# Kernel tuning notes

Measured on AMD Instinct MI355X. Metric: run time of the kernel, lower is better.

## Reference

```python
import jax, jax.numpy as jnp
import numpy as np

B = 64          # number of jets
LVLS = 13       # tree levels (complete binary tree, 4096 leaves/jet)
F = 7           # input features
H = 64          # hidden size
SIZES = [B * (2 ** j) for j in range(LVLS)]
OFFS = np.concatenate([[0], np.cumsum(SIZES)])  # level offsets into flat contents


def setup_inputs() -> dict:
    key = jax.random.key(0)
    ks = jax.random.split(key, 9)
    n_total = int(OFFS[-1])  # 524224
    s = lambda k, shp, fan: jax.random.normal(k, shp, jnp.float32) / np.sqrt(fan)
    return {
        "contents": jax.random.normal(ks[0], (n_total, F), jnp.float32),
        "W_u": s(ks[1], (H, F), F),       "b_u": jnp.zeros((H,), jnp.float32),
        "W_r": s(ks[2], (3 * H, 3 * H), 3 * H), "b_r": jnp.zeros((3 * H,), jnp.float32),
        "W_h": s(ks[3], (H, 3 * H), 3 * H),     "b_h": jnp.zeros((H,), jnp.float32),
        "W_z": s(ks[4], (4 * H, 4 * H), 4 * H), "b_z": jnp.zeros((4 * H,), jnp.float32),
    }


def reference(contents, W_u, b_u, W_r, b_r, W_h, b_h, W_z, b_z):
    # Bottom-up recursive gated embedding (n_iters=0 path -> relu activation).
    up = None  # embedding of level j+1
    for j in reversed(range(LVLS)):
        c = contents[int(OFFS[j]):int(OFFS[j + 1])]        # [n_j, F]
        u = jax.nn.relu(c @ W_u.T + b_u)                   # [n_j, H]
        if j == LVLS - 1:
            up = u                                         # leaf level: no inners
            continue
        n = SIZES[j]
        # children of node k are (2k, 2k+1) at level j+1 -> strided gather
        h_L = up[0::2]                                     # [n_j, H]
        h_R = up[1::2]                                     # [n_j, H]
        hhu = jnp.concatenate([h_L, h_R, u], axis=1)       # [n_j, 3H]
        r = jax.nn.sigmoid(hhu @ W_r.T + b_r)              # reset gate
        h_H = jax.nn.relu((r * hhu) @ W_h.T + b_h)         # candidate
        z = jnp.concatenate([h_H, hhu], axis=1) @ W_z.T + b_z  # [n_j, 4H]
        g = jax.nn.softmax(z.reshape(n, 4, H), axis=1)     # softmax over 4 gates
        up = g[:, 0] * h_H + g[:, 1] * h_L + g[:, 2] * h_R + g[:, 3] * u
    return up.reshape(B, -1)                               # [B, H]
```

## Files before the change

### kernel.cpp

```cpp
#include <hip/hip_runtime.h>
#include <hip/hip_bf16.h>


#define LOG2E 1.4426950408889634f
#define OSTR 76

typedef __bf16 bf16x8 __attribute__((ext_vector_type(8)));
typedef float f32x4 __attribute__((ext_vector_type(4)));
typedef unsigned short bfr;

__device__ __forceinline__ float bfr2f(bfr v) { return __uint_as_float(((unsigned)v) << 16); }
__device__ __forceinline__ bfr f2bfr(float f) {
    __hip_bfloat16 h = __float2bfloat16(f);
    return __builtin_bit_cast(bfr, h);
}
__device__ __forceinline__ float fexp2(float x) {
#if __has_builtin(__builtin_amdgcn_exp2f)
    return __builtin_amdgcn_exp2f(x);
#else
    return exp2f(x);
#endif
}
__device__ __forceinline__ float frcp(float x) {
#if __has_builtin(__builtin_amdgcn_rcpf)
    return __builtin_amdgcn_rcpf(x);
#else
    return 1.f / x;
#endif
}

__device__ __forceinline__ int fidx(int Mt, int kt, int q, int ln, int KT) {
    return ((((Mt * KT + kt) * 4 + q) * 16 + ln) * 8);
}

__device__ __host__ __forceinline__ size_t lvloff(int j) {
    return (size_t)((64 << j) - 64) * 64;
}

__device__ __forceinline__ void pack_one(const float* __restrict__ W, bfr* __restrict__ dst,
                                         int d, int K, float scale) {
    int KT = K >> 5;
    int j = d & 7, lnc = (d >> 3) & 15, q = (d >> 7) & 3;
    int t1 = d >> 9;
    int kt = t1 % KT, ntile = t1 / KT;
    int ncol = ntile * 16 + lnc;
    int k = kt * 32 + q * 8 + j;
    dst[d] = f2bfr(W[(size_t)ncol * K + k] * scale);
}

__global__ void convert_weights(const float* __restrict__ Wr, const float* __restrict__ Wh,
                                const float* __restrict__ Wz, const float* __restrict__ Wu,
                                const float* __restrict__ br, const float* __restrict__ bz,
                                bfr* __restrict__ wr, bfr* __restrict__ wh, bfr* __restrict__ wz,
                                bfr* __restrict__ wu,
                                float* __restrict__ brs, float* __restrict__ bzs) {
    int i = blockIdx.x * 256 + threadIdx.x;
    if (i < 36864) pack_one(Wr, wr, i, 192, LOG2E);
    if (i < 12288) pack_one(Wh, wh, i, 192, 1.f);
    if (i < 65536) pack_one(Wz, wz, i, 256, LOG2E);
    if (i < 2048) {
        int j = i & 7, lnc = (i >> 3) & 15, q = (i >> 7) & 3, ntile = i >> 9;
        int k = q * 8 + j, ncol = ntile * 16 + lnc;
        wu[i] = (k < 7) ? f2bfr(Wu[ncol * 7 + k]) : (bfr)0;
    }
    if (i < 192) brs[i] = br[i] * LOG2E;
    if (i < 256) bzs[i] = bz[i] * LOG2E;
}

__device__ __forceinline__ void stage_c(const float* __restrict__ csrc, int rows,
                                        bfr* s_c) {
    const int tid = threadIdx.x;
    for (int t = tid; t < rows * 4; t += 256) {
        int row = t >> 2, qg = t & 3;
        ushort v[8] = {0, 0, 0, 0, 0, 0, 0, 0};
        if (qg == 0) {
            const float* cp = csrc + (size_t)row * 7;
#pragma unroll
            for (int k = 0; k < 7; ++k) v[k] = f2bfr(cp[k]);
        }
        *(uint4*)&s_c[(((row >> 4) * 4 + qg) * 16 + (row & 15)) * 8] = *(const uint4*)v;
    }
}

__device__ __forceinline__ void store_up_coalesced(
    int row0, int rows, bfr* __restrict__ u_io,
    const ushort (&ovv)[4][4], int Mtn, bfr* s_t)
{
    const int tid = threadIdx.x;
    const int lane = tid & 63, w = tid >> 6;
    const int ln = lane & 15, q = lane >> 4;
    const int colbase = w * 16 + q * 4;
    __syncthreads();
#pragma unroll
    for (int Mt = 0; Mt < 4; ++Mt) {
        if (Mt < Mtn) {
            int row = Mt * 16 + ln;
            if (row < rows)
                *(uint2*)&s_t[row * OSTR + colbase] = *(const uint2*)ovv[Mt];
        }
    }
    __syncthreads();
#pragma unroll
    for (int it = 0; it < 2; ++it) {
        int idx = it * 256 + tid;
        int row = idx >> 3, ck = idx & 7;
        if (row < rows)
            *(uint4*)&u_io[(size_t)(row0 + row) * 64 + ck * 8] =
                *(const uint4*)&s_t[row * OSTR + ck * 8];
    }
}

__device__ __forceinline__ void mmu_own(const bfr* s_c, bfr* s_hhu, bf16x8 awu,
                                        f32x4 bu4, int Mtn, int ln, int q,
                                        int colbase) {
#pragma unroll
    for (int Mt = 0; Mt < 4; ++Mt) {
        if (Mt < Mtn) {
            bf16x8 Bc = *(const bf16x8*)&s_c[((Mt * 4 + q) * 16 + ln) * 8];
            f32x4 acc = {0.f, 0.f, 0.f, 0.f};
            acc = __builtin_amdgcn_mfma_f32_16x16x32_bf16(awu, Bc, acc, 0, 0, 0);
            int kk = 128 + colbase;
            int addr = fidx(Mt, kk >> 5, (kk >> 3) & 3, ln, 6) + (kk & 7);
            ushort uv[4];
#pragma unroll
            for (int r = 0; r < 4; ++r) uv[r] = f2bfr(fmaxf(acc[r] + bu4[r], 0.f));
            *(uint2*)&s_hhu[addr] = *(const uint2*)uv;
        }
    }
}

template <bool CHILD_U>
__device__ __forceinline__ void process_level_glob(
    int row0,
    const bfr* __restrict__ ch, const float* __restrict__ c_child,
    const float* __restrict__ c_own, bfr* __restrict__ u_io,
    const bfr* __restrict__ wu, const float* __restrict__ b_u,
    const bfr* __restrict__ wr, const float* __restrict__ brs,
    const bfr* __restrict__ wh, const float* __restrict__ b_h,
    const bfr* __restrict__ wz, const float* __restrict__ bzs,
    bfr* s_hhu, bfr* s_t)
{
    bfr* s_hH = s_t;
    const int tid = threadIdx.x;
    const int lane = tid & 63, w = tid >> 6;
    const int ln = lane & 15, q = lane >> 4;
    const int colbase = w * 16 + q * 4;
    const int rows = 64, Mtn = 4;

    if (!CHILD_U) {
#pragma unroll
        for (int it = 0; it < 4; ++it) {
            int idx = it * 256 + tid;
            int lns = idx & 15, qs = (idx >> 4) & 3, kts = (idx >> 6) & 3, Mts = idx >> 8;
            int row = Mts * 16 + lns;
            int k = kts * 32 + qs * 8;
            const bfr* src = (k < 64)
                ? ch + (size_t)(2 * (row0 + row)) * 64 + k
                : ch + (size_t)(2 * (row0 + row) + 1) * 64 + (k - 64);
            *(uint4*)&s_hhu[fidx(Mts, kts, qs, lns, 6)] = *(const uint4*)src;
        }
    } else {
        stage_c(c_child + (size_t)(2 * row0) * 7, 128, s_t + 2048);
    }
    stage_c(c_own + (size_t)row0 * 7, 64, s_t);
    __syncthreads();

    {
        bf16x8 awu = *(const bf16x8*)&wu[fidx(w, 0, q, ln, 1)];
        f32x4 bu4 = *(const f32x4*)&b_u[colbase];
        if (CHILD_U) {
#pragma unroll
            for (int Mt = 0; Mt < 8; ++Mt) {
                bf16x8 Bc = *(const bf16x8*)&s_t[2048 + (((Mt * 4 + q) * 16 + ln) * 8)];
                f32x4 acc = {0.f, 0.f, 0.f, 0.f};
                acc = __builtin_amdgcn_mfma_f32_16x16x32_bf16(awu, Bc, acc, 0, 0, 0);
                int crow = Mt * 16 + ln;
                int row = crow >> 1;
                int kk = (crow & 1) * 64 + colbase;
                int addr = fidx(row >> 4, kk >> 5, (kk >> 3) & 3, row & 15, 6) + (kk & 7);
                ushort uv[4];
#pragma unroll
                for (int r = 0; r < 4; ++r) uv[r] = f2bfr(fmaxf(acc[r] + bu4[r], 0.f));
                *(uint2*)&s_hhu[addr] = *(const uint2*)uv;
            }
        }
        mmu_own(s_t, s_hhu, awu, bu4, 4, ln, q, colbase);
    }
    __syncthreads();

    {
        bf16x8 Af[3][6];
#pragma unroll
        for (int nt = 0; nt < 3; ++nt)
#pragma unroll
            for (int kt = 0; kt < 6; ++kt)
                Af[nt][kt] = *(const bf16x8*)&wr[fidx(w * 3 + nt, kt, q, ln, 6)];
#pragma unroll
        for (int Mt = 0; Mt < 4; ++Mt) {
            bf16x8 Bf[6];
#pragma unroll
            for (int kt = 0; kt < 6; ++kt)
                Bf[kt] = *(const bf16x8*)&s_hhu[fidx(Mt, kt, q, ln, 6)];
#pragma unroll
            for (int nt = 0; nt < 3; ++nt) {
                int cb1 = (w * 3 + nt) * 16 + q * 4;
                f32x4 acc = {0.f, 0.f, 0.f, 0.f};
#pragma unroll
                for (int kt = 0; kt < 6; ++kt)
                    acc = __builtin_amdgcn_mfma_f32_16x16x32_bf16(Af[nt][kt], Bf[kt], acc, 0, 0, 0);
                f32x4 br4 = *(const f32x4*)&brs[cb1];
                int addr = fidx(Mt, cb1 >> 5, (cb1 >> 3) & 3, ln, 6) + (cb1 & 7);
                ushort hh[4], tt[4];
                *(uint2*)hh = *(const uint2*)&s_hhu[addr];
#pragma unroll
                for (int r = 0; r < 4; ++r) {
                    float e = fexp2(-(acc[r] + br4[r]));
                    tt[r] = f2bfr(frcp(1.f + e) * bfr2f(hh[r]));
                }
                *(uint2*)&s_t[addr] = *(const uint2*)tt;
            }
        }
    }
    __syncthreads();

    f32x4 hacc[4];
    {
        bf16x8 Ah[6];
#pragma unroll
        for (int kt = 0; kt < 6; ++kt)
            Ah[kt] = *(const bf16x8*)&wh[fidx(w, kt, q, ln, 6)];
#pragma unroll
        for (int Mt = 0; Mt < 4; ++Mt) {
            f32x4 acc = {0.f, 0.f, 0.f, 0.f};
#pragma unroll
            for (int kt = 0; kt < 6; ++kt) {
                bf16x8 Bf = *(const bf16x8*)&s_t[fidx(Mt, kt, q, ln, 6)];
                acc = __builtin_amdgcn_mfma_f32_16x16x32_bf16(Ah[kt], Bf, acc, 0, 0, 0);
            }
            hacc[Mt] = acc;
        }
    }
    __syncthreads();
    {
        f32x4 bh4 = *(const f32x4*)&b_h[colbase];
#pragma unroll
        for (int Mt = 0; Mt < 4; ++Mt) {
            int addr = fidx(Mt, colbase >> 5, (colbase >> 3) & 3, ln, 2) + (colbase & 7);
            ushort hv[4];
#pragma unroll
            for (int r = 0; r < 4; ++r) hv[r] = f2bfr(fmaxf(hacc[Mt][r] + bh4[r], 0.f));
            *(uint2*)&s_hH[addr] = *(const uint2*)hv;
        }
    }
    __syncthreads();

    {
        f32x4 az[4][4];
#pragma unroll
        for (int Mt = 0; Mt < 4; ++Mt)
#pragma unroll
            for (int g = 0; g < 4; ++g) az[Mt][g] = (f32x4){0.f, 0.f, 0.f, 0.f};
#pragma unroll
        for (int g = 0; g < 4; ++g) {
            bf16x8 Aw[8];
#pragma unroll
            for (int kt = 0; kt < 8; ++kt)
                Aw[kt] = *(const bf16x8*)&wz[fidx(g * 4 + w, kt, q, ln, 8)];
#pragma unroll
            for (int Mt = 0; Mt < 4; ++Mt) {
                f32x4 acc = az[Mt][g];
                acc = __builtin_amdgcn_mfma_f32_16x16x32_bf16(
                    Aw[0], *(const bf16x8*)&s_hH[fidx(Mt, 0, q, ln, 2)], acc, 0, 0, 0);
                acc = __builtin_amdgcn_mfma_f32_16x16x32_bf16(
                    Aw[1], *(const bf16x8*)&s_hH[fidx(Mt, 1, q, ln, 2)], acc, 0, 0, 0);
#pragma unroll
                for (int kt = 0; kt < 6; ++kt)
                    acc = __builtin_amdgcn_mfma_f32_16x16x32_bf16(
                        Aw[2 + kt], *(const bf16x8*)&s_hhu[fidx(Mt, kt, q, ln, 6)], acc, 0, 0, 0);
                az[Mt][g] = acc;
            }
        }
        f32x4 bz0 = *(const f32x4*)&bzs[colbase];
        f32x4 bz1 = *(const f32x4*)&bzs[64 + colbase];
        f32x4 bz2 = *(const f32x4*)&bzs[128 + colbase];
        f32x4 bz3 = *(const f32x4*)&bzs[192 + colbase];
        ushort ovv[4][4];
#pragma unroll
        for (int Mt = 0; Mt < 4; ++Mt) {
            int aH = fidx(Mt, colbase >> 5, (colbase >> 3) & 3, ln, 2) + (colbase & 7);
            int a0 = fidx(Mt, colbase >> 5, (colbase >> 3) & 3, ln, 6) + (colbase & 7);
            int c1 = 64 + colbase, c2 = 128 + colbase;
            int a1 = fidx(Mt, c1 >> 5, (c1 >> 3) & 3, ln, 6) + (c1 & 7);
            int a2 = fidx(Mt, c2 >> 5, (c2 >> 3) & 3, ln, 6) + (c2 & 7);
            ushort hHv[4], u0[4], u1[4], u2[4];
            *(uint2*)hHv = *(const uint2*)&s_hH[aH];
            *(uint2*)u0 = *(const uint2*)&s_hhu[a0];
            *(uint2*)u1 = *(const uint2*)&s_hhu[a1];
            *(uint2*)u2 = *(const uint2*)&s_hhu[a2];
#pragma unroll
            for (int r = 0; r < 4; ++r) {
                float e0 = fexp2(az[Mt][0][r] + bz0[r]);
                float e1 = fexp2(az[Mt][1][r] + bz1[r]);
                float e2 = fexp2(az[Mt][2][r] + bz2[r]);
                float e3 = fexp2(az[Mt][3][r] + bz3[r]);
                float inv = frcp(e0 + e1 + e2 + e3);
                float v = (e0 * bfr2f(hHv[r]) + e1 * bfr2f(u0[r]) +
                           e2 * bfr2f(u1[r]) + e3 * bfr2f(u2[r])) * inv;
                ovv[Mt][r] = f2bfr(v);
            }
        }
        store_up_coalesced(row0, rows, u_io, ovv, Mtn, s_t);
    }
}

__global__ __launch_bounds__(256, 2) void level11_kernel(
    const float* __restrict__ c12, const float* __restrict__ c11,
    bfr* __restrict__ u_io,
    const bfr* __restrict__ wr, const float* __restrict__ brs,
    const bfr* __restrict__ wh, const float* __restrict__ b_h,
    const bfr* __restrict__ wz, const float* __restrict__ bzs,
    const bfr* __restrict__ wu, const float* __restrict__ b_u)
{
    __shared__ bfr s_hhu[12288];
    __shared__ bfr s_t[12288];
    process_level_glob<true>(blockIdx.x * 64, nullptr, c12, c11, u_io,
                             wu, b_u, wr, brs, wh, b_h, wz, bzs, s_hhu, s_t);
}

__global__ __launch_bounds__(256, 2) void level_kernel(
    const bfr* __restrict__ ch, const float* __restrict__ c_own,
    bfr* __restrict__ u_io,
    const bfr* __restrict__ wr, const float* __restrict__ brs,
    const bfr* __restrict__ wh, const float* __restrict__ b_h,
    const bfr* __restrict__ wz, const float* __restrict__ bzs,
    const bfr* __restrict__ wu, const float* __restrict__ b_u)
{
    __shared__ bfr s_hhu[12288];
    __shared__ bfr s_t[12288];
    process_level_glob<false>(blockIdx.x * 64, ch, nullptr, c_own, u_io,
                              wu, b_u, wr, brs, wh, b_h, wz, bzs, s_hhu, s_t);
}

__device__ __forceinline__ void load_wregs(
    const bfr* __restrict__ wr, const bfr* __restrict__ wh, const bfr* __restrict__ wz,
    const bfr* __restrict__ wu, int w, int q, int ln,
    bf16x8 (&Af)[3][6], bf16x8 (&Ah)[6], bf16x8 (&Aw)[4][8], bf16x8& awu)
{
#pragma unroll
    for (int nt = 0; nt < 3; ++nt)
#pragma unroll
        for (int kt = 0; kt < 6; ++kt)
            Af[nt][kt] = *(const bf16x8*)&wr[fidx(w * 3 + nt, kt, q, ln, 6)];
#pragma unroll
    for (int kt = 0; kt < 6; ++kt)
        Ah[kt] = *(const bf16x8*)&wh[fidx(w, kt, q, ln, 6)];
#pragma unroll
    for (int g = 0; g < 4; ++g)
#pragma unroll
        for (int kt = 0; kt < 8; ++kt)
            Aw[g][kt] = *(const bf16x8*)&wz[fidx(g * 4 + w, kt, q, ln, 8)];
    awu = *(const bf16x8*)&wu[fidx(w, 0, q, ln, 1)];
}

__device__ __forceinline__ void process_level_regs(
    int row0, int rows,
    const bfr* __restrict__ ch, const float* __restrict__ c_own,
    bfr* __restrict__ u_io,
    const bf16x8 awu, const float* __restrict__ b_u,
    const bf16x8 (&Af)[3][6], const bf16x8 (&Ah)[6], const bf16x8 (&Aw)[4][8],
    const float* __restrict__ brs, const float* __restrict__ b_h,
    const float* __restrict__ bzs,
    float* __restrict__ outp, bfr* s_hhu, bfr* s_t)
{
    bfr* s_hH = s_t;
    const int tid = threadIdx.x;
    const int lane = tid & 63, w = tid >> 6;
    const int ln = lane & 15, q = lane >> 4;
    const int Mtn = (rows + 15) >> 4;
    const int colbase = w * 16 + q * 4;

    __syncthreads();

#pragma unroll
    for (int it = 0; it < 4; ++it) {
        int idx = it * 256 + tid;
        int lns = idx & 15, qs = (idx >> 4) & 3, kts = (idx >> 6) & 3, Mts = idx >> 8;
        int row = Mts * 16 + lns;
        if (row < rows) {
            int k = kts * 32 + qs * 8;
            const bfr* src = (k < 64)
                ? ch + (size_t)(2 * (row0 + row)) * 64 + k
                : ch + (size_t)(2 * (row0 + row) + 1) * 64 + (k - 64);
            *(uint4*)&s_hhu[fidx(Mts, kts, qs, lns, 6)] = *(const uint4*)src;
        }
    }
    stage_c(c_own + (size_t)row0 * 7, rows, s_t);
    __syncthreads();

    {
        f32x4 bu4 = *(const f32x4*)&b_u[colbase];
        mmu_own(s_t, s_hhu, awu, bu4, Mtn, ln, q, colbase);
    }
    __syncthreads();

#pragma unroll
    for (int Mt = 0; Mt < 4; ++Mt) {
        if (Mt < Mtn) {
            bf16x8 Bf[6];
#pragma unroll
            for (int kt = 0; kt < 6; ++kt)
                Bf[kt] = *(const bf16x8*)&s_hhu[fidx(Mt, kt, q, ln, 6)];
#pragma unroll
            for (int nt = 0; nt < 3; ++nt) {
                int cb1 = (w * 3 + nt) * 16 + q * 4;
                f32x4 acc = {0.f, 0.f, 0.f, 0.f};
#pragma unroll
                for (int kt = 0; kt < 6; ++kt)
                    acc = __builtin_amdgcn_mfma_f32_16x16x32_bf16(Af[nt][kt], Bf[kt], acc, 0, 0, 0);
                f32x4 br4 = *(const f32x4*)&brs[cb1];
                int addr = fidx(Mt, cb1 >> 5, (cb1 >> 3) & 3, ln, 6) + (cb1 & 7);
                ushort hh[4], tt[4];
                *(uint2*)hh = *(const uint2*)&s_hhu[addr];
#pragma unroll
                for (int r = 0; r < 4; ++r) {
                    float e = fexp2(-(acc[r] + br4[r]));
                    tt[r] = f2bfr(frcp(1.f + e) * bfr2f(hh[r]));
                }
                *(uint2*)&s_t[addr] = *(const uint2*)tt;
            }
        }
    }
    __syncthreads();

    f32x4 hacc[4];
#pragma unroll
    for (int Mt = 0; Mt < 4; ++Mt) {
        if (Mt < Mtn) {
            f32x4 acc = {0.f, 0.f, 0.f, 0.f};
#pragma unroll
            for (int kt = 0; kt < 6; ++kt) {
                bf16x8 Bf = *(const bf16x8*)&s_t[fidx(Mt, kt, q, ln, 6)];
                acc = __builtin_amdgcn_mfma_f32_16x16x32_bf16(Ah[kt], Bf, acc, 0, 0, 0);
            }
            hacc[Mt] = acc;
        }
    }
    __syncthreads();
    {
        f32x4 bh4 = *(const f32x4*)&b_h[colbase];
#pragma unroll
        for (int Mt = 0; Mt < 4; ++Mt) {
            if (Mt < Mtn) {
                int addr = fidx(Mt, colbase >> 5, (colbase >> 3) & 3, ln, 2) + (colbase & 7);
                ushort hv[4];
#pragma unroll
                for (int r = 0; r < 4; ++r) hv[r] = f2bfr(fmaxf(hacc[Mt][r] + bh4[r], 0.f));
                *(uint2*)&s_hH[addr] = *(const uint2*)hv;
            }
        }
    }
    __syncthreads();

    {
        f32x4 bz0 = *(const f32x4*)&bzs[colbase];
        f32x4 bz1 = *(const f32x4*)&bzs[64 + colbase];
        f32x4 bz2 = *(const f32x4*)&bzs[128 + colbase];
        f32x4 bz3 = *(const f32x4*)&bzs[192 + colbase];
        ushort ovv[4][4];
#pragma unroll
        for (int Mt = 0; Mt < 4; ++Mt) {
            if (Mt < Mtn) {
                bf16x8 Az[8];
                Az[0] = *(const bf16x8*)&s_hH[fidx(Mt, 0, q, ln, 2)];
                Az[1] = *(const bf16x8*)&s_hH[fidx(Mt, 1, q, ln, 2)];
#pragma unroll
                for (int kt = 0; kt < 6; ++kt)
                    Az[2 + kt] = *(const bf16x8*)&s_hhu[fidx(Mt, kt, q, ln, 6)];
                f32x4 azg[4];
#pragma unroll
                for (int g = 0; g < 4; ++g) {
                    f32x4 acc = {0.f, 0.f, 0.f, 0.f};
#pragma unroll
                    for (int kt = 0; kt < 8; ++kt)
                        acc = __builtin_amdgcn_mfma_f32_16x16x32_bf16(Aw[g][kt], Az[kt], acc, 0, 0, 0);
                    azg[g] = acc;
                }
                int aH = fidx(Mt, colbase >> 5, (colbase >> 3) & 3, ln, 2) + (colbase & 7);
                int a0 = fidx(Mt, colbase >> 5, (colbase >> 3) & 3, ln, 6) + (colbase & 7);
                int c1 = 64 + colbase, c2 = 128 + colbase;
                int a1 = fidx(Mt, c1 >> 5, (c1 >> 3) & 3, ln, 6) + (c1 & 7);
                int a2 = fidx(Mt, c2 >> 5, (c2 >> 3) & 3, ln, 6) + (c2 & 7);
                int row = Mt * 16 + ln;
                if (row < rows) {
                    ushort hHv[4], u0[4], u1[4], u2[4];
                    *(uint2*)hHv = *(const uint2*)&s_hH[aH];
                    *(uint2*)u0 = *(const uint2*)&s_hhu[a0];
                    *(uint2*)u1 = *(const uint2*)&s_hhu[a1];
                    *(uint2*)u2 = *(const uint2*)&s_hhu[a2];
                    float of[4];
#pragma unroll
                    for (int r = 0; r < 4; ++r) {
                        float e0 = fexp2(azg[0][r] + bz0[r]);
                        float e1 = fexp2(azg[1][r] + bz1[r]);
                        float e2 = fexp2(azg[2][r] + bz2[r]);
                        float e3 = fexp2(azg[3][r] + bz3[r]);
                        float inv = frcp(e0 + e1 + e2 + e3);
                        float v = (e0 * bfr2f(hHv[r]) + e1 * bfr2f(u0[r]) +
                                   e2 * bfr2f(u1[r]) + e3 * bfr2f(u2[r])) * inv;
                        ovv[Mt][r] = f2bfr(v); of[r] = v;
                    }
                    if (outp)
                        *(float4*)&outp[(size_t)(row0 + row) * 64 + colbase] = *(const float4*)of;
                }
            }
        }
        store_up_coalesced(row0, rows, u_io, ovv, Mtn, s_t);
    }
}

__global__ __launch_bounds__(256, 1) void fused_mid_regs(
    const float* __restrict__ contents, bfr* __restrict__ u_all,
    const bfr* __restrict__ wr, const float* __restrict__ brs,
    const bfr* __restrict__ wh, const float* __restrict__ b_h,
    const bfr* __restrict__ wz, const float* __restrict__ bzs,
    const bfr* __restrict__ wu, const float* __restrict__ b_u)
{
    __shared__ bfr s_hhu[12288];
    __shared__ bfr s_t[12288];
    const int tid = threadIdx.x;
    const int lane = tid & 63, w = tid >> 6, ln = lane & 15, q = lane >> 4;
    bf16x8 Af[3][6], Ah[6], Aw[4][8], awu;
    load_wregs(wr, wh, wz, wu, w, q, ln, Af, Ah, Aw, awu);
    for (int j = 8; j >= 2; --j) {
        int rows = 1 << (j - 2);
        const float* c_own = contents + (size_t)((64 << j) - 64) * 7;
        process_level_regs(blockIdx.x * rows, rows,
                           u_all + lvloff(j + 1), c_own, u_all + lvloff(j),
                           awu, b_u, Af, Ah, Aw, brs, b_h, bzs,
                           nullptr, s_hhu, s_t);
    }
}

__global__ __launch_bounds__(256, 1) void fused_tail_regs(
    const float* __restrict__ contents, bfr* __restrict__ u_all,
    const bfr* __restrict__ wr, const float* __restrict__ brs,
    const bfr* __restrict__ wh, const float* __restrict__ b_h,
    const bfr* __restrict__ wz, const float* __restrict__ bzs,
    const bfr* __restrict__ wu, const float* __restrict__ b_u,
    float* __restrict__ outp)
{
    __shared__ bfr s_hhu[12288];
    __shared__ bfr s_t[12288];
    const int tid = threadIdx.x;
    const int lane = tid & 63, w = tid >> 6, ln = lane & 15, q = lane >> 4;
    bf16x8 Af[3][6], Ah[6], Aw[4][8], awu;
    load_wregs(wr, wh, wz, wu, w, q, ln, Af, Ah, Aw, awu);
    for (int j = 1; j >= 0; --j) {
        int rows = 1 << j;
        const float* c_own = contents + (size_t)((64 << j) - 64) * 7;
        process_level_regs(blockIdx.x * rows, rows,
                           u_all + lvloff(j + 1), c_own, u_all + lvloff(j),
                           awu, b_u, Af, Ah, Aw, brs, b_h, bzs,
                           (j == 0) ? outp : nullptr, s_hhu, s_t);
    }
}

extern "C" void kernel_launch(void* const* d_in, const int* in_sizes, int n_in,
                              void* d_out, int out_size, void* d_ws, size_t ws_size,
                              hipStream_t stream) {
    const float* contents = (const float*)d_in[0];
    const float* W_u = (const float*)d_in[1];
    const float* b_u = (const float*)d_in[2];
    const float* W_r = (const float*)d_in[3];
    const float* b_r = (const float*)d_in[4];
    const float* W_h = (const float*)d_in[5];
    const float* b_h = (const float*)d_in[6];
    const float* W_z = (const float*)d_in[7];
    const float* b_z = (const float*)d_in[8];
    float* out = (float*)d_out;

    bfr* u_all = (bfr*)d_ws;
    bfr* wr = u_all + (size_t)524224 * 64;
    bfr* wh = wr + 36864;
    bfr* wz = wh + 12288;
    float* brs = (float*)(wz + 65536);
    float* bzs = brs + 192;
    bfr* wu = (bfr*)(bzs + 256);

    convert_weights<<<256, 256, 0, stream>>>(W_r, W_h, W_z, W_u, b_r, b_z,
                                             wr, wh, wz, wu, brs, bzs);

    const float* c12 = contents + (size_t)((64 << 12) - 64) * 7;
    const float* c11 = contents + (size_t)((64 << 11) - 64) * 7;
    const float* c10 = contents + (size_t)((64 << 10) - 64) * 7;
    const float* c9  = contents + (size_t)((64 << 9) - 64) * 7;

    level11_kernel<<<2048, 256, 0, stream>>>(c12, c11, u_all + lvloff(11),
                                             wr, brs, wh, b_h, wz, bzs, wu, b_u);
    level_kernel<<<1024, 256, 0, stream>>>(u_all + lvloff(11), c10, u_all + lvloff(10),
                                           wr, brs, wh, b_h, wz, bzs, wu, b_u);
    level_kernel<<<512, 256, 0, stream>>>(u_all + lvloff(10), c9, u_all + lvloff(9),
                                          wr, brs, wh, b_h, wz, bzs, wu, b_u);
    fused_mid_regs<<<256, 256, 0, stream>>>(contents, u_all,
                                            wr, brs, wh, b_h, wz, bzs, wu, b_u);
    fused_tail_regs<<<64, 256, 0, stream>>>(contents, u_all,
                                            wr, brs, wh, b_h, wz, bzs, wu, b_u, out);
}
```

Measured before the change: 199.0 us.

## Load contents fragments directly into MFMA registers and drop extra barriers

Leaf and own-node feature rows are now read from global memory straight into MFMA B-fragments instead of being staged through shared memory. That removes a staging pass and its barrier. A separate shared buffer for h_H lets the W_h matmul write its result immediately instead of holding accumulators across an extra __syncthreads. The output tile is written to shared memory in the epilogue itself, which removes one more barrier before the coalesced store. Each level pass needs fewer block-wide syncs, at the cost of more LDS and uncoalesced 7-float reads per lane.

```diff
diff --git a/kernel.cpp b/kernel.cpp
--- a/kernel.cpp
+++ b/kernel.cpp
@@ -6,6 +6,7 @@
 #define OSTR 76
 
 typedef __bf16 bf16x8 __attribute__((ext_vector_type(8)));
+typedef unsigned short u16x8 __attribute__((ext_vector_type(8)));
 typedef float f32x4 __attribute__((ext_vector_type(4)));
 typedef unsigned short bfr;
 
@@ -67,39 +68,20 @@
     if (i < 256) bzs[i] = bz[i] * LOG2E;
 }
 
-__device__ __forceinline__ void stage_c(const float* __restrict__ csrc, int rows,
-                                        bfr* s_c) {
+__device__ __forceinline__ bf16x8 load_c_frag(const float* __restrict__ c,
+                                              size_t grow, bool active) {
+    u16x8 cv = {0, 0, 0, 0, 0, 0, 0, 0};
+    if (active) {
+        const float* cp = c + grow * 7;
+#pragma unroll
+        for (int k = 0; k < 7; ++k) cv[k] = f2bfr(cp[k]);
+    }
+    return __builtin_bit_cast(bf16x8, cv);
+}
+
+__device__ __forceinline__ void coop_store(int row0, int rows,
+                                           bfr* __restrict__ u_io, const bfr* s_t) {
     const int tid = threadIdx.x;
-    for (int t = tid; t < rows * 4; t += 256) {
-        int row = t >> 2, qg = t & 3;
-        ushort v[8] = {0, 0, 0, 0, 0, 0, 0, 0};
-        if (qg == 0) {
-            const float* cp = csrc + (size_t)row * 7;
-#pragma unroll
-            for (int k = 0; k < 7; ++k) v[k] = f2bfr(cp[k]);
-        }
-        *(uint4*)&s_c[(((row >> 4) * 4 + qg) * 16 + (row & 15)) * 8] = *(const uint4*)v;
-    }
-}
-
-__device__ __forceinline__ void store_up_coalesced(
-    int row0, int rows, bfr* __restrict__ u_io,
-    const ushort (&ovv)[4][4], int Mtn, bfr* s_t)
-{
-    const int tid = threadIdx.x;
-    const int lane = tid & 63, w = tid >> 6;
-    const int ln = lane & 15, q = lane >> 4;
-    const int colbase = w * 16 + q * 4;
-    __syncthreads();
-#pragma unroll
-    for (int Mt = 0; Mt < 4; ++Mt) {
-        if (Mt < Mtn) {
-            int row = Mt * 16 + ln;
-            if (row < rows)
-                *(uint2*)&s_t[row * OSTR + colbase] = *(const uint2*)ovv[Mt];
-        }
-    }
-    __syncthreads();
 #pragma unroll
     for (int it = 0; it < 2; ++it) {
         int idx = it * 256 + tid;
@@ -110,60 +92,22 @@
     }
 }
 
-__device__ __forceinline__ void mmu_own(const bfr* s_c, bfr* s_hhu, bf16x8 awu,
-                                        f32x4 bu4, int Mtn, int ln, int q,
-                                        int colbase) {
-#pragma unroll
-    for (int Mt = 0; Mt < 4; ++Mt) {
-        if (Mt < Mtn) {
-            bf16x8 Bc = *(const bf16x8*)&s_c[((Mt * 4 + q) * 16 + ln) * 8];
-            f32x4 acc = {0.f, 0.f, 0.f, 0.f};
-            acc = __builtin_amdgcn_mfma_f32_16x16x32_bf16(awu, Bc, acc, 0, 0, 0);
-            int kk = 128 + colbase;
-            int addr = fidx(Mt, kk >> 5, (kk >> 3) & 3, ln, 6) + (kk & 7);
-            ushort uv[4];
-#pragma unroll
-            for (int r = 0; r < 4; ++r) uv[r] = f2bfr(fmaxf(acc[r] + bu4[r], 0.f));
-            *(uint2*)&s_hhu[addr] = *(const uint2*)uv;
-        }
-    }
-}
-
 template <bool CHILD_U>
-__device__ __forceinline__ void process_level_glob(
-    int row0,
+__device__ __forceinline__ void tile_glob(
+    int row0, int rows,
     const bfr* __restrict__ ch, const float* __restrict__ c_child,
     const float* __restrict__ c_own, bfr* __restrict__ u_io,
     const bfr* __restrict__ wu, const float* __restrict__ b_u,
     const bfr* __restrict__ wr, const float* __restrict__ brs,
     const bfr* __restrict__ wh, const float* __restrict__ b_h,
     const bfr* __restrict__ wz, const float* __restrict__ bzs,
-    bfr* s_hhu, bfr* s_t)
-{
-    bfr* s_hH = s_t;
+    bfr* s_hhu, bfr* s_t, bfr* s_hH)
+{
     const int tid = threadIdx.x;
     const int lane = tid & 63, w = tid >> 6;
     const int ln = lane & 15, q = lane >> 4;
     const int colbase = w * 16 + q * 4;
-    const int rows = 64, Mtn = 4;
-
-    if (!CHILD_U) {
-#pragma unroll
-        for (int it = 0; it < 4; ++it) {
-            int idx = it * 256 + tid;
-            int lns = idx & 15, qs = (idx >> 4) & 3, kts = (idx >> 6) & 3, Mts = idx >> 8;
-            int row = Mts * 16 + lns;
-            int k = kts * 32 + qs * 8;
-            const bfr* src = (k < 64)
-                ? ch + (size_t)(2 * (row0 + row)) * 64 + k
-                : ch + (size_t)(2 * (row0 + row) + 1) * 64 + (k - 64);
-            *(uint4*)&s_hhu[fidx(Mts, kts, qs, lns, 6)] = *(const uint4*)src;
-        }
-    } else {
-        stage_c(c_child + (size_t)(2 * row0) * 7, 128, s_t + 2048);
-    }
-    stage_c(c_own + (size_t)row0 * 7, 64, s_t);
-    __syncthreads();
+    const int Mtn = (rows + 15) >> 4;
 
     {
         bf16x8 awu = *(const bf16x8*)&wu[fidx(w, 0, q, ln, 1)];
@@ -171,10 +115,10 @@
         if (CHILD_U) {
 #pragma unroll
             for (int Mt = 0; Mt < 8; ++Mt) {
-                bf16x8 Bc = *(const bf16x8*)&s_t[2048 + (((Mt * 4 + q) * 16 + ln) * 8)];
+                int crow = Mt * 16 + ln;
+                bf16x8 Bc = load_c_frag(c_child, (size_t)(2 * row0) + crow, q == 0);
                 f32x4 acc = {0.f, 0.f, 0.f, 0.f};
                 acc = __builtin_amdgcn_mfma_f32_16x16x32_bf16(awu, Bc, acc, 0, 0, 0);
-                int crow = Mt * 16 + ln;
                 int row = crow >> 1;
                 int kk = (crow & 1) * 64 + colbase;
                 int addr = fidx(row >> 4, kk >> 5, (kk >> 3) & 3, row & 15, 6) + (kk & 7);
@@ -183,8 +127,36 @@
                 for (int r = 0; r < 4; ++r) uv[r] = f2bfr(fmaxf(acc[r] + bu4[r], 0.f));
                 *(uint2*)&s_hhu[addr] = *(const uint2*)uv;
             }
-        }
-        mmu_own(s_t, s_hhu, awu, bu4, 4, ln, q, colbase);
+        } else {
+#pragma unroll
+            for (int it = 0; it < 4; ++it) {
+                int idx = it * 256 + tid;
+                int lns = idx & 15, qs = (idx >> 4) & 3, kts = (idx >> 6) & 3, Mts = idx >> 8;
+                int row = Mts * 16 + lns;
+                if (row < rows) {
+                    int k = kts * 32 + qs * 8;
+                    const bfr* src = (k < 64)
+                        ? ch + (size_t)(2 * (row0 + row)) * 64 + k
+                        : ch + (size_t)(2 * (row0 + row) + 1) * 64 + (k - 64);
+                    *(uint4*)&s_hhu[fidx(Mts, kts, qs, lns, 6)] = *(const uint4*)src;
+                }
+            }
+        }
+#pragma unroll
+        for (int Mt = 0; Mt < 4; ++Mt) {
+            if (Mt < Mtn) {
+                int row = Mt * 16 + ln;
+                bf16x8 Bc = load_c_frag(c_own, (size_t)row0 + row, q == 0 && row < rows);
+                f32x4 acc = {0.f, 0.f, 0.f, 0.f};
+                acc = __builtin_amdgcn_mfma_f32_16x16x32_bf16(awu, Bc, acc, 0, 0, 0);
+                int kk = 128 + colbase;
+                int addr = fidx(Mt, kk >> 5, (kk >> 3) & 3, ln, 6) + (kk & 7);
+                ushort uv[4];
+#pragma unroll
+                for (int r = 0; r < 4; ++r) uv[r] = f2bfr(fmaxf(acc[r] + bu4[r], 0.f));
+                *(uint2*)&s_hhu[addr] = *(const uint2*)uv;
+            }
+        }
     }
     __syncthreads();
 
@@ -197,59 +169,55 @@
                 Af[nt][kt] = *(const bf16x8*)&wr[fidx(w * 3 + nt, kt, q, ln, 6)];
 #pragma unroll
         for (int Mt = 0; Mt < 4; ++Mt) {
-            bf16x8 Bf[6];
-#pragma unroll
-            for (int kt = 0; kt < 6; ++kt)
-                Bf[kt] = *(const bf16x8*)&s_hhu[fidx(Mt, kt, q, ln, 6)];
-#pragma unroll
-            for (int nt = 0; nt < 3; ++nt) {
-                int cb1 = (w * 3 + nt) * 16 + q * 4;
-                f32x4 acc = {0.f, 0.f, 0.f, 0.f};
+            if (Mt < Mtn) {
+                bf16x8 Bf[6];
 #pragma unroll
                 for (int kt = 0; kt < 6; ++kt)
-                    acc = __builtin_amdgcn_mfma_f32_16x16x32_bf16(Af[nt][kt], Bf[kt], acc, 0, 0, 0);
-                f32x4 br4 = *(const f32x4*)&brs[cb1];
-                int addr = fidx(Mt, cb1 >> 5, (cb1 >> 3) & 3, ln, 6) + (cb1 & 7);
-                ushort hh[4], tt[4];
-                *(uint2*)hh = *(const uint2*)&s_hhu[addr];
-#pragma unroll
-                for (int r = 0; r < 4; ++r) {
-                    float e = fexp2(-(acc[r] + br4[r]));
-                    tt[r] = f2bfr(frcp(1.f + e) * bfr2f(hh[r]));
-                }
-                *(uint2*)&s_t[addr] = *(const uint2*)tt;
-            }
-        }
-    }
-    __syncthreads();
-
-    f32x4 hacc[4];
+                    Bf[kt] = *(const bf16x8*)&s_hhu[fidx(Mt, kt, q, ln, 6)];
+#pragma unroll
+                for (int nt = 0; nt < 3; ++nt) {
+                    int cb1 = (w * 3 + nt) * 16 + q * 4;
+                    f32x4 acc = {0.f, 0.f, 0.f, 0.f};
+#pragma unroll
+                    for (int kt = 0; kt < 6; ++kt)
+                        acc = __builtin_amdgcn_mfma_f32_16x16x32_bf16(Af[nt][kt], Bf[kt], acc, 0, 0, 0);
+                    f32x4 br4 = *(const f32x4*)&brs[cb1];
+                    int addr = fidx(Mt, cb1 >> 5, (cb1 >> 3) & 3, ln, 6) + (cb1 & 7);
+                    ushort hh[4], tt[4];
+                    *(uint2*)hh = *(const uint2*)&s_hhu[addr];
+#pragma unroll
+                    for (int r = 0; r < 4; ++r) {
+                        float e = fexp2(-(acc[r] + br4[r]));
+                        tt[r] = f2bfr(frcp(1.f + e) * bfr2f(hh[r]));
+                    }
+                    *(uint2*)&s_t[addr] = *(const uint2*)tt;
+                }
+            }
+        }
+    }
+    __syncthreads();
+
     {
         bf16x8 Ah[6];
 #pragma unroll
         for (int kt = 0; kt < 6; ++kt)
             Ah[kt] = *(const bf16x8*)&wh[fidx(w, kt, q, ln, 6)];
-#pragma unroll
-        for (int Mt = 0; Mt < 4; ++Mt) {
-            f32x4 acc = {0.f, 0.f, 0.f, 0.f};
-#pragma unroll
-            for (int kt = 0; kt < 6; ++kt) {
-                bf16x8 Bf = *(const bf16x8*)&s_t[fidx(Mt, kt, q, ln, 6)];
-                acc = __builtin_amdgcn_mfma_f32_16x16x32_bf16(Ah[kt], Bf, acc, 0, 0, 0);
-            }
-            hacc[Mt] = acc;
-        }
-    }
-    __syncthreads();
-    {
         f32x4 bh4 = *(const f32x4*)&b_h[colbase];
 #pragma unroll
         for (int Mt = 0; Mt < 4; ++Mt) {
-            int addr = fidx(Mt, colbase >> 5, (colbase >> 3) & 3, ln, 2) + (colbase & 7);
-            ushort hv[4];
-#pragma unroll
-            for (int r = 0; r < 4; ++r) hv[r] = f2bfr(fmaxf(hacc[Mt][r] + bh4[r], 0.f));
-            *(uint2*)&s_hH[addr] = *(const uint2*)hv;
+            if (Mt < Mtn) {
+                f32x4 acc = {0.f, 0.f, 0.f, 0.f};
+#pragma unroll
+                for (int kt = 0; kt < 6; ++kt) {
+                    bf16x8 Bf = *(const bf16x8*)&s_t[fidx(Mt, kt, q, ln, 6)];
+                    acc = __builtin_amdgcn_mfma_f32_16x16x32_bf16(Ah[kt], Bf, acc, 0, 0, 0);
+                }
+                int addr = fidx(Mt, colbase >> 5, (colbase >> 3) & 3, ln, 2) + (colbase & 7);
+                ushort hv[4];
+#pragma unroll
+                for (int r = 0; r < 4; ++r) hv[r] = f2bfr(fmaxf(acc[r] + bh4[r], 0.f));
+                *(uint2*)&s_hH[addr] = *(const uint2*)hv;
+            }
         }
     }
     __syncthreads();
@@ -268,49 +236,57 @@
                 Aw[kt] = *(const bf16x8*)&wz[fidx(g * 4 + w, kt, q, ln, 8)];
 #pragma unroll
             for (int Mt = 0; Mt < 4; ++Mt) {
-                f32x4 acc = az[Mt][g];
-                acc = __builtin_amdgcn_mfma_f32_16x16x32_bf16(
-                    Aw[0], *(const bf16x8*)&s_hH[fidx(Mt, 0, q, ln, 2)], acc, 0, 0, 0);
-                acc = __builtin_amdgcn_mfma_f32_16x16x32_bf16(
-                    Aw[1], *(const bf16x8*)&s_hH[fidx(Mt, 1, q, ln, 2)], acc, 0, 0, 0);
-#pragma unroll
-                for (int kt = 0; kt < 6; ++kt)
+                if (Mt < Mtn) {
+                    f32x4 acc = az[Mt][g];
                     acc = __builtin_amdgcn_mfma_f32_16x16x32_bf16(
-                        Aw[2 + kt], *(const bf16x8*)&s_hhu[fidx(Mt, kt, q, ln, 6)], acc, 0, 0, 0);
-                az[Mt][g] = acc;
+                        Aw[0], *(const bf16x8*)&s_hH[fidx(Mt, 0, q, ln, 2)], acc, 0, 0, 0);
+                    acc = __builtin_amdgcn_mfma_f32_16x16x32_bf16(
+                        Aw[1], *(const bf16x8*)&s_hH[fidx(Mt, 1, q, ln, 2)], acc, 0, 0, 0);
+#pragma unroll
+                    for (int kt = 0; kt < 6; ++kt)
+                        acc = __builtin_amdgcn_mfma_f32_16x16x32_bf16(
+                            Aw[2 + kt], *(const bf16x8*)&s_hhu[fidx(Mt, kt, q, ln, 6)], acc, 0, 0, 0);
+                    az[Mt][g] = acc;
+                }
             }
         }
         f32x4 bz0 = *(const f32x4*)&bzs[colbase];
         f32x4 bz1 = *(const f32x4*)&bzs[64 + colbase];
         f32x4 bz2 = *(const f32x4*)&bzs[128 + colbase];
         f32x4 bz3 = *(const f32x4*)&bzs[192 + colbase];
-        ushort ovv[4][4];
-#pragma unroll
-        for (int Mt = 0; Mt < 4; ++Mt) {
-            int aH = fidx(Mt, colbase >> 5, (colbase >> 3) & 3, ln, 2) + (colbase & 7);
-            int a0 = fidx(Mt, colbase >> 5, (colbase >> 3) & 3, ln, 6) + (colbase & 7);
-            int c1 = 64 + colbase, c2 = 128 + colbase;
-            int a1 = fidx(Mt, c1 >> 5, (c1 >> 3) & 3, ln, 6) + (c1 & 7);
-            int a2 = fidx(Mt, c2 >> 5, (c2 >> 3) & 3, ln, 6) + (c2 & 7);
-            ushort hHv[4], u0[4], u1[4], u2[4];
-            *(uint2*)hHv = *(const uint2*)&s_hH[aH];
-            *(uint2*)u0 = *(const uint2*)&s_hhu[a0];
-            *(uint2*)u1 = *(const uint2*)&s_hhu[a1];
-            *(uint2*)u2 = *(const uint2*)&s_hhu[a2];
-#pragma unroll
-            for (int r = 0; r < 4; ++r) {
-                float e0 = fexp2(az[Mt][0][r] + bz0[r]);
-                float e1 = fexp2(az[Mt][1][r] + bz1[r]);
-                float e2 = fexp2(az[Mt][2][r] + bz2[r]);
-                float e3 = fexp2(az[Mt][3][r] + bz3[r]);
-                float inv = frcp(e0 + e1 + e2 + e3);
-                float v = (e0 * bfr2f(hHv[r]) + e1 * bfr2f(u0[r]) +
-                           e2 * bfr2f(u1[r]) + e3 * bfr2f(u2[r])) * inv;
-                ovv[Mt][r] = f2bfr(v);
-            }
-        }
-        store_up_coalesced(row0, rows, u_io, ovv, Mtn, s_t);
-    }
+#pragma unroll
+        for (int Mt = 0; Mt < 4; ++Mt) {
+            if (Mt < Mtn) {
+                int row = Mt * 16 + ln;
+                if (row < rows) {
+                    int aH = fidx(Mt, colbase >> 5, (colbase >> 3) & 3, ln, 2) + (colbase & 7);
+                    int a0 = fidx(Mt, colbase >> 5, (colbase >> 3) & 3, ln, 6) + (colbase & 7);
+                    int c1 = 64 + colbase, c2 = 128 + colbase;
+                    int a1 = fidx(Mt, c1 >> 5, (c1 >> 3) & 3, ln, 6) + (c1 & 7);
+                    int a2 = fidx(Mt, c2 >> 5, (c2 >> 3) & 3, ln, 6) + (c2 & 7);
+                    ushort hHv[4], u0[4], u1[4], u2[4], ov[4];
+                    *(uint2*)hHv = *(const uint2*)&s_hH[aH];
+                    *(uint2*)u0 = *(const uint2*)&s_hhu[a0];
+                    *(uint2*)u1 = *(const uint2*)&s_hhu[a1];
+                    *(uint2*)u2 = *(const uint2*)&s_hhu[a2];
+#pragma unroll
+                    for (int r = 0; r < 4; ++r) {
+                        float e0 = fexp2(az[Mt][0][r] + bz0[r]);
+                        float e1 = fexp2(az[Mt][1][r] + bz1[r]);
+                        float e2 = fexp2(az[Mt][2][r] + bz2[r]);
+                        float e3 = fexp2(az[Mt][3][r] + bz3[r]);
+                        float inv = frcp(e0 + e1 + e2 + e3);
+                        float v = (e0 * bfr2f(hHv[r]) + e1 * bfr2f(u0[r]) +
+                                   e2 * bfr2f(u1[r]) + e3 * bfr2f(u2[r])) * inv;
+                        ov[r] = f2bfr(v);
+                    }
+                    *(uint2*)&s_t[row * OSTR + colbase] = *(const uint2*)ov;
+                }
+            }
+        }
+    }
+    __syncthreads();
+    coop_store(row0, rows, u_io, s_t);
 }
 
 __global__ __launch_bounds__(256, 2) void level11_kernel(
@@ -323,8 +299,9 @@
 {
     __shared__ bfr s_hhu[12288];
     __shared__ bfr s_t[12288];
-    process_level_glob<true>(blockIdx.x * 64, nullptr, c12, c11, u_io,
-                             wu, b_u, wr, brs, wh, b_h, wz, bzs, s_hhu, s_t);
+    __shared__ bfr s_hH[4096];
+    tile_glob<true>(blockIdx.x * 64, 64, nullptr, c12, c11, u_io,
+                    wu, b_u, wr, brs, wh, b_h, wz, bzs, s_hhu, s_t, s_hH);
 }
 
 __global__ __launch_bounds__(256, 2) void level_kernel(
@@ -337,8 +314,9 @@
 {
     __shared__ bfr s_hhu[12288];
     __shared__ bfr s_t[12288];
-    process_level_glob<false>(blockIdx.x * 64, ch, nullptr, c_own, u_io,
-                              wu, b_u, wr, brs, wh, b_h, wz, bzs, s_hhu, s_t);
+    __shared__ bfr s_hH[4096];
+    tile_glob<false>(blockIdx.x * 64, 64, ch, nullptr, c_own, u_io,
+                     wu, b_u, wr, brs, wh, b_h, wz, bzs, s_hhu, s_t, s_hH);
 }
 
 __device__ __forceinline__ void load_wregs(
@@ -362,7 +340,7 @@
     awu = *(const bf16x8*)&wu[fidx(w, 0, q, ln, 1)];
 }
 
-__device__ __forceinline__ void process_level_regs(
+__device__ __forceinline__ void tile_regs(
     int row0, int rows,
     const bfr* __restrict__ ch, const float* __restrict__ c_own,
     bfr* __restrict__ u_io,
@@ -370,9 +348,8 @@
     const bf16x8 (&Af)[3][6], const bf16x8 (&Ah)[6], const bf16x8 (&Aw)[4][8],
     const float* __restrict__ brs, const float* __restrict__ b_h,
     const float* __restrict__ bzs,
-    float* __restrict__ outp, bfr* s_hhu, bfr* s_t)
-{
-    bfr* s_hH = s_t;
+    float* __restrict__ outp, bfr* s_hhu, bfr* s_t, bfr* s_hH)
+{
     const int tid = threadIdx.x;
     const int lane = tid & 63, w = tid >> 6;
     const int ln = lane & 15, q = lane >> 4;
@@ -394,12 +371,23 @@
             *(uint4*)&s_hhu[fidx(Mts, kts, qs, lns, 6)] = *(const uint4*)src;
         }
     }
-    stage_c(c_own + (size_t)row0 * 7, rows, s_t);
-    __syncthreads();
-
     {
         f32x4 bu4 = *(const f32x4*)&b_u[colbase];
-        mmu_own(s_t, s_hhu, awu, bu4, Mtn, ln, q, colbase);
+#pragma unroll
+        for (int Mt = 0; Mt < 4; ++Mt) {
+            if (Mt < Mtn) {
+                int row = Mt * 16 + ln;
+                bf16x8 Bc = load_c_frag(c_own, (size_t)row0 + row, q == 0 && row < rows);
+                f32x4 acc = {0.f, 0.f, 0.f, 0.f};
+                acc = __builtin_amdgcn_mfma_f32_16x16x32_bf16(awu, Bc, acc, 0, 0, 0);
+                int kk = 128 + colbase;
+                int addr = fidx(Mt, kk >> 5, (kk >> 3) & 3, ln, 6) + (kk & 7);
+                ushort uv[4];
+#pragma unroll
+                for (int r = 0; r < 4; ++r) uv[r] = f2bfr(fmaxf(acc[r] + bu4[r], 0.f));
+                *(uint2*)&s_hhu[addr] = *(const uint2*)uv;
+            }
+        }
     }
     __syncthreads();
 
@@ -432,29 +420,21 @@
     }
     __syncthreads();
 
-    f32x4 hacc[4];
-#pragma unroll
-    for (int Mt = 0; Mt < 4; ++Mt) {
-        if (Mt < Mtn) {
-            f32x4 acc = {0.f, 0.f, 0.f, 0.f};
-#pragma unroll
-            for (int kt = 0; kt < 6; ++kt) {
-                bf16x8 Bf = *(const bf16x8*)&s_t[fidx(Mt, kt, q, ln, 6)];
-                acc = __builtin_amdgcn_mfma_f32_16x16x32_bf16(Ah[kt], Bf, acc, 0, 0, 0);
-            }
-            hacc[Mt] = acc;
-        }
-    }
-    __syncthreads();
     {
         f32x4 bh4 = *(const f32x4*)&b_h[colbase];
 #pragma unroll
         for (int Mt = 0; Mt < 4; ++Mt) {
             if (Mt < Mtn) {
+                f32x4 acc = {0.f, 0.f, 0.f, 0.f};
+#pragma unroll
+                for (int kt = 0; kt < 6; ++kt) {
+                    bf16x8 Bf = *(const bf16x8*)&s_t[fidx(Mt, kt, q, ln, 6)];
+                    acc = __builtin_amdgcn_mfma_f32_16x16x32_bf16(Ah[kt], Bf, acc, 0, 0, 0);
+                }
                 int addr = fidx(Mt, colbase >> 5, (colbase >> 3) & 3, ln, 2) + (colbase & 7);
                 ushort hv[4];
 #pragma unroll
-                for (int r = 0; r < 4; ++r) hv[r] = f2bfr(fmaxf(hacc[Mt][r] + bh4[r], 0.f));
+                for (int r = 0; r < 4; ++r) hv[r] = f2bfr(fmaxf(acc[r] + bh4[r], 0.f));
                 *(uint2*)&s_hH[addr] = *(const uint2*)hv;
             }
         }
@@ -466,7 +446,6 @@
         f32x4 bz1 = *(const f32x4*)&bzs[64 + colbase];
         f32x4 bz2 = *(const f32x4*)&bzs[128 + colbase];
         f32x4 bz3 = *(const f32x4*)&bzs[192 + colbase];
-        ushort ovv[4][4];
 #pragma unroll
         for (int Mt = 0; Mt < 4; ++Mt) {
             if (Mt < Mtn) {
@@ -485,14 +464,14 @@
                         acc = __builtin_amdgcn_mfma_f32_16x16x32_bf16(Aw[g][kt], Az[kt], acc, 0, 0, 0);
                     azg[g] = acc;
                 }
-                int aH = fidx(Mt, colbase >> 5, (colbase >> 3) & 3, ln, 2) + (colbase & 7);
-                int a0 = fidx(Mt, colbase >> 5, (colbase >> 3) & 3, ln, 6) + (colbase & 7);
-                int c1 = 64 + colbase, c2 = 128 + colbase;
-                int a1 = fidx(Mt, c1 >> 5, (c1 >> 3) & 3, ln, 6) + (c1 & 7);
-                int a2 = fidx(Mt, c2 >> 5, (c2 >> 3) & 3, ln, 6) + (c2 & 7);
                 int row = Mt * 16 + ln;
                 if (row < rows) {
-                    ushort hHv[4], u0[4], u1[4], u2[4];
+                    int aH = fidx(Mt, colbase >> 5, (colbase >> 3) & 3, ln, 2) + (colbase & 7);
+                    int a0 = fidx(Mt, colbase >> 5, (colbase >> 3) & 3, ln, 6) + (colbase & 7);
+                    int c1 = 64 + colbase, c2 = 128 + colbase;
+                    int a1 = fidx(Mt, c1 >> 5, (c1 >> 3) & 3, ln, 6) + (c1 & 7);
+                    int a2 = fidx(Mt, c2 >> 5, (c2 >> 3) & 3, ln, 6) + (c2 & 7);
+                    ushort hHv[4], u0[4], u1[4], u2[4], ov[4];
                     *(uint2*)hHv = *(const uint2*)&s_hH[aH];
                     *(uint2*)u0 = *(const uint2*)&s_hhu[a0];
                     *(uint2*)u1 = *(const uint2*)&s_hhu[a1];
@@ -507,15 +486,17 @@
                         float inv = frcp(e0 + e1 + e2 + e3);
                         float v = (e0 * bfr2f(hHv[r]) + e1 * bfr2f(u0[r]) +
                                    e2 * bfr2f(u1[r]) + e3 * bfr2f(u2[r])) * inv;
-                        ovv[Mt][r] = f2bfr(v); of[r] = v;
+                        ov[r] = f2bfr(v); of[r] = v;
                     }
+                    *(uint2*)&s_t[row * OSTR + colbase] = *(const uint2*)ov;
                     if (outp)
                         *(float4*)&outp[(size_t)(row0 + row) * 64 + colbase] = *(const float4*)of;
                 }
             }
         }
-        store_up_coalesced(row0, rows, u_io, ovv, Mtn, s_t);
-    }
+    }
+    __syncthreads();
+    coop_store(row0, rows, u_io, s_t);
 }
 
 __global__ __launch_bounds__(256, 1) void fused_mid_regs(
@@ -527,6 +508,7 @@
 {
     __shared__ bfr s_hhu[12288];
     __shared__ bfr s_t[12288];
+    __shared__ bfr s_hH[4096];
     const int tid = threadIdx.x;
     const int lane = tid & 63, w = tid >> 6, ln = lane & 15, q = lane >> 4;
     bf16x8 Af[3][6], Ah[6], Aw[4][8], awu;
@@ -534,10 +516,10 @@
     for (int j = 8; j >= 2; --j) {
         int rows = 1 << (j - 2);
         const float* c_own = contents + (size_t)((64 << j) - 64) * 7;
-        process_level_regs(blockIdx.x * rows, rows,
-                           u_all + lvloff(j + 1), c_own, u_all + lvloff(j),
-                           awu, b_u, Af, Ah, Aw, brs, b_h, bzs,
-                           nullptr, s_hhu, s_t);
+        tile_regs(blockIdx.x * rows, rows,
+                  u_all + lvloff(j + 1), c_own, u_all + lvloff(j),
+                  awu, b_u, Af, Ah, Aw, brs, b_h, bzs,
+                  nullptr, s_hhu, s_t, s_hH);
     }
 }
 
@@ -551,6 +533,7 @@
 {
     __shared__ bfr s_hhu[12288];
     __shared__ bfr s_t[12288];
+    __shared__ bfr s_hH[4096];
     const int tid = threadIdx.x;
     const int lane = tid & 63, w = tid >> 6, ln = lane & 15, q = lane >> 4;
     bf16x8 Af[3][6], Ah[6], Aw[4][8], awu;
@@ -558,10 +541,10 @@
     for (int j = 1; j >= 0; --j) {
         int rows = 1 << j;
         const float* c_own = contents + (size_t)((64 << j) - 64) * 7;
-        process_level_regs(blockIdx.x * rows, rows,
-                           u_all + lvloff(j + 1), c_own, u_all + lvloff(j),
-                           awu, b_u, Af, Ah, Aw, brs, b_h, bzs,
-                           (j == 0) ? outp : nullptr, s_hhu, s_t);
+        tile_regs(blockIdx.x * rows, rows,
+                  u_all + lvloff(j + 1), c_own, u_all + lvloff(j),
+                  awu, b_u, Af, Ah, Aw, brs, b_h, bzs,
+                  (j == 0) ? outp : nullptr, s_hhu, s_t, s_hH);
     }
 }
 
```

Result: slower. 203.6 us (+2.3%).
